# Kernel tuning notes

Hardware: AMD Instinct MI355X
Metric: run time of the kernel (lower is better)

Reference implementation:

```python
import jax, jax.numpy as jnp
import numpy as np

FP8_MAX = 448.0  # e4m3
EPS = 1e-12


def setup_inputs() -> dict:
    key = jax.random.key(0)
    k1, k2, k3 = jax.random.split(key, 3)
    x = jax.random.normal(k1, (4, 4096, 2048), dtype=jnp.float32)
    weight = jax.random.normal(k2, (2048, 2048), dtype=jnp.float32) * 0.02
    bias = jax.random.normal(k3, (2048,), dtype=jnp.float32) * 0.01
    return {"x": x, "weight": weight, "bias": bias}


def reference(x, weight, bias):
    # Per-tensor input quantization (fake FP8 e4m3)
    input_amax = jnp.max(jnp.abs(x))
    input_scale = jnp.maximum(input_amax / FP8_MAX, EPS)
    x_q = jnp.round(jnp.clip(x / input_scale, -FP8_MAX, FP8_MAX))

    # Per-output-channel weight quantization (margin = 0.0 default)
    w_amax = jnp.max(jnp.abs(weight), axis=1)              # [out]
    w_scale = jnp.maximum(w_amax / FP8_MAX, EPS)            # [out]
    w_q = jnp.round(jnp.clip(weight / w_scale[:, None], -FP8_MAX, FP8_MAX))

    # GEMM on quantized values, then dequantize with combined scales
    out_q = jnp.einsum('bsi,oi->bso', x_q, w_q)             # [b, s, out]
    out = out_q * (input_scale * w_scale)                   # broadcast over out
    return out + bias
```

## Files before the change

### kernel.cpp

```cpp
#include <hip/hip_runtime.h>
#include <cstdint>
#include <cstddef>

#define FP8_MAX 448.0f
#define KDIM 2048
#define NDIM 2048

typedef _Float16 half8 __attribute__((ext_vector_type(8)));
typedef float floatx4 __attribute__((ext_vector_type(4)));

__device__ __forceinline__ float fabs4max(float4 v) {
  return fmaxf(fmaxf(fabsf(v.x), fabsf(v.y)), fmaxf(fabsf(v.z), fabsf(v.w)));
}

__device__ __forceinline__ _Float16 quant1(float v, float inv) {
  return (_Float16)rintf(fminf(fmaxf(v * inv, -FP8_MAX), FP8_MAX));
}

__device__ __forceinline__ void gload_lds16(const void* g, void* l) {
  __builtin_amdgcn_global_load_lds(
      (const __attribute__((address_space(1))) unsigned int*)g,
      (__attribute__((address_space(3))) unsigned int*)l,
      16, 0, 0);
}

__global__ __launch_bounds__(256) void k_amax(const float4* __restrict__ x4, int n4,
                                              float* __restrict__ partial) {
  float m = 0.f;
  int stride = gridDim.x * blockDim.x;
  for (int i = blockIdx.x * blockDim.x + threadIdx.x; i < n4; i += stride)
    m = fmaxf(m, fabs4max(x4[i]));
#pragma unroll
  for (int off = 32; off > 0; off >>= 1)
    m = fmaxf(m, __shfl_xor(m, off));
  __shared__ float red[4];
  if ((threadIdx.x & 63) == 0) red[threadIdx.x >> 6] = m;
  __syncthreads();
  if (threadIdx.x == 0)
    partial[blockIdx.x] = fmaxf(fmaxf(red[0], red[1]), fmaxf(red[2], red[3]));
}

__global__ __launch_bounds__(256) void k_amax2(const float* __restrict__ partial, int n,
                                               float* __restrict__ amax) {
  int t = threadIdx.x;
  float m = 0.f;
  for (int i = t; i < n; i += 256) m = fmaxf(m, partial[i]);
#pragma unroll
  for (int off = 32; off > 0; off >>= 1)
    m = fmaxf(m, __shfl_xor(m, off));
  __shared__ float red[4];
  if ((t & 63) == 0) red[t >> 6] = m;
  __syncthreads();
  if (t == 0) amax[0] = fmaxf(fmaxf(red[0], red[1]), fmaxf(red[2], red[3]));
}

__global__ __launch_bounds__(256) void k_xquant(const float4* __restrict__ x4,
                                                const float* __restrict__ amax,
                                                half8* __restrict__ xq, int n8) {
  float scale = fmaxf(amax[0] / FP8_MAX, 1e-12f);
  float inv = 1.f / scale;
  int stride = gridDim.x * blockDim.x;
  for (int i = blockIdx.x * blockDim.x + threadIdx.x; i < n8; i += stride) {
    float4 a = x4[2 * i];
    float4 b = x4[2 * i + 1];
    half8 q;
    q[0] = quant1(a.x, inv); q[1] = quant1(a.y, inv);
    q[2] = quant1(a.z, inv); q[3] = quant1(a.w, inv);
    q[4] = quant1(b.x, inv); q[5] = quant1(b.y, inv);
    q[6] = quant1(b.z, inv); q[7] = quant1(b.w, inv);
    xq[i] = q;
  }
}

__global__ __launch_bounds__(256) void k_wquant(const float* __restrict__ w,
                                                const float* __restrict__ amax,
                                                _Float16* __restrict__ wq,
                                                float* __restrict__ comb) {
  int row = blockIdx.x;
  int t = threadIdx.x;
  const float4* w4 = (const float4*)(w + (size_t)row * KDIM);
  float4 a = w4[2 * t];
  float4 b = w4[2 * t + 1];
  float m = fmaxf(fabs4max(a), fabs4max(b));
#pragma unroll
  for (int off = 32; off > 0; off >>= 1)
    m = fmaxf(m, __shfl_xor(m, off));
  __shared__ float red[4];
  if ((t & 63) == 0) red[t >> 6] = m;
  __syncthreads();
  float rowmax = fmaxf(fmaxf(red[0], red[1]), fmaxf(red[2], red[3]));
  float wscale = fmaxf(rowmax / FP8_MAX, 1e-12f);
  float inv = 1.f / wscale;
  half8 q;
  q[0] = quant1(a.x, inv); q[1] = quant1(a.y, inv);
  q[2] = quant1(a.z, inv); q[3] = quant1(a.w, inv);
  q[4] = quant1(b.x, inv); q[5] = quant1(b.y, inv);
  q[6] = quant1(b.z, inv); q[7] = quant1(b.w, inv);
  *(half8*)(wq + (size_t)row * KDIM + t * 8) = q;
  if (t == 0) {
    float iscale = fmaxf(amax[0] / FP8_MAX, 1e-12f);
    comb[row] = iscale * wscale;
  }
}

__global__ __launch_bounds__(512, 2) void k_gemm256(const _Float16* __restrict__ A,
                                                    const _Float16* __restrict__ B,
                                                    const float* __restrict__ comb,
                                                    const float* __restrict__ bias,
                                                    float* __restrict__ C, int M) {
  __shared__ _Float16 smem[3 * 16384];

  const int NT = KDIM / 32;
  int nwg = gridDim.x;
  int bid = blockIdx.x;
  int swz = bid;
  if ((nwg & 7) == 0) {
    int cpx = nwg >> 3;
    swz = (bid & 7) * cpx + (bid >> 3);
  }
  const int NBN = NDIM / 256;
  int bm = swz / NBN, bn = swz % NBN;

  int tid = threadIdx.x;
  int lane = tid & 63;
  int w = tid >> 6;
  int wr = w >> 2;
  int wc = w & 3;

  int sR = tid >> 2;
  int sc = (tid & 3) ^ ((tid >> 3) & 3);
  const _Float16* gA = A + (size_t)bm * 256 * KDIM;
  const _Float16* gB = B + (size_t)bn * 256 * KDIM;
  size_t off0 = (size_t)sR * KDIM + sc * 8;
  size_t off1 = (size_t)(sR + 128) * KDIM + sc * 8;

  int g = lane >> 4;
  int lr = lane & 15;
  int gx = g ^ ((lr >> 1) & 3);
  int aOff = (wr * 128 + lr) * 64 + gx * 16;
  int bOff = (wc * 64 + lr) * 64 + gx * 16;

  const floatx4 zero4 = {0.f, 0.f, 0.f, 0.f};
  floatx4 acc[8][4];
#pragma unroll
  for (int i = 0; i < 8; ++i)
#pragma unroll
    for (int j = 0; j < 4; ++j) acc[i][j] = zero4;

#define STAGE_A(t, buf)                                                        \
  do {                                                                         \
    const _Float16* src = gA + (size_t)(t)*32;                                 \
    char* dst = (char*)smem + (buf)*32768;                                     \
    gload_lds16(src + off0, dst + tid * 16);                                   \
    gload_lds16(src + off1, dst + 8192 + tid * 16);                            \
  } while (0)
#define STAGE_B(t, buf)                                                        \
  do {                                                                         \
    const _Float16* src = gB + (size_t)(t)*32;                                 \
    char* dst = (char*)smem + (buf)*32768 + 16384;                             \
    gload_lds16(src + off0, dst + tid * 16);                                   \
    gload_lds16(src + off1, dst + 8192 + tid * 16);                            \
  } while (0)

  STAGE_A(0, 0); STAGE_B(0, 0);
  STAGE_A(1, 1); STAGE_B(1, 1);
  asm volatile("s_waitcnt vmcnt(4)" ::: "memory");
  __builtin_amdgcn_s_barrier();

  half8 af[4], bf[4];
  for (int t = 0; t < NT; ++t) {
    int buf = t % 3;
    const char* Abuf = (const char*)smem + buf * 32768;
    const char* Bbuf = Abuf + 16384;
    int nbuf = (t + 2) % 3;
    bool do_stage = (t + 2 < NT);

#pragma unroll
    for (int n = 0; n < 4; ++n) bf[n] = *(const half8*)(Bbuf + bOff + n * 1024);
#pragma unroll
    for (int m = 0; m < 4; ++m) af[m] = *(const half8*)(Abuf + aOff + m * 1024);
    if (do_stage) STAGE_A(t + 2, nbuf);
    __builtin_amdgcn_s_setprio(1);
#pragma unroll
    for (int m = 0; m < 4; ++m)
#pragma unroll
      for (int n = 0; n < 4; ++n)
        acc[m][n] = __builtin_amdgcn_mfma_f32_16x16x32_f16(af[m], bf[n], acc[m][n], 0, 0, 0);
    __builtin_amdgcn_s_setprio(0);
    __builtin_amdgcn_s_barrier();

#pragma unroll
    for (int m = 0; m < 4; ++m) af[m] = *(const half8*)(Abuf + aOff + 4096 + m * 1024);
    if (do_stage) STAGE_B(t + 2, nbuf);
    __builtin_amdgcn_s_setprio(1);
#pragma unroll
    for (int m = 0; m < 4; ++m)
#pragma unroll
      for (int n = 0; n < 4; ++n)
        acc[4 + m][n] = __builtin_amdgcn_mfma_f32_16x16x32_f16(af[m], bf[n], acc[4 + m][n], 0, 0, 0);
    __builtin_amdgcn_s_setprio(0);

    asm volatile("s_waitcnt lgkmcnt(0)" ::: "memory");
    if (t < NT - 2)
      asm volatile("s_waitcnt vmcnt(4)" ::: "memory");
    else
      asm volatile("s_waitcnt vmcnt(0)" ::: "memory");
    __builtin_amdgcn_s_barrier();
  }
#undef STAGE_A
#undef STAGE_B

  int cbase = bn * 256 + wc * 64 + (lane & 15);
  float s[4], bv[4];
#pragma unroll
  for (int n = 0; n < 4; ++n) {
    s[n] = comb[cbase + n * 16];
    bv[n] = bias[cbase + n * 16];
  }
#pragma unroll
  for (int mh = 0; mh < 2; ++mh)
#pragma unroll
    for (int m = 0; m < 4; ++m) {
      size_t row = (size_t)bm * 256 + wr * 128 + mh * 64 + m * 16 + ((lane >> 4) << 2);
      float* cp = C + row * NDIM + cbase;
#pragma unroll
      for (int n = 0; n < 4; ++n)
#pragma unroll
        for (int j = 0; j < 4; ++j)
          cp[n * 16 + (size_t)j * NDIM] = acc[mh * 4 + m][n][j] * s[n] + bv[n];
    }
}

extern "C" void kernel_launch(void* const* d_in, const int* in_sizes, int n_in,
                              void* d_out, int out_size, void* d_ws, size_t ws_size,
                              hipStream_t stream) {
  const float* x = (const float*)d_in[0];
  const float* w = (const float*)d_in[1];
  const float* bias = (const float*)d_in[2];
  float* out = (float*)d_out;
  int M = in_sizes[0] / KDIM;

  char* ws = (char*)d_ws;
  size_t xq_bytes = (size_t)in_sizes[0] * sizeof(_Float16);
  size_t wq_bytes = (size_t)in_sizes[1] * sizeof(_Float16);
  _Float16* xq = (_Float16*)ws;
  _Float16* wq = (_Float16*)(ws + xq_bytes);
  float* comb = (float*)(ws + xq_bytes + wq_bytes);
  float* amax = (float*)(ws + xq_bytes + wq_bytes + 8192);
  float* partial = (float*)(ws + xq_bytes + wq_bytes + 8192 + 256);

  const int AMAX_BLOCKS = 2048;
  int n4 = in_sizes[0] / 4;
  k_amax<<<AMAX_BLOCKS, 256, 0, stream>>>((const float4*)x, n4, partial);
  k_amax2<<<1, 256, 0, stream>>>(partial, AMAX_BLOCKS, amax);

  int n8 = in_sizes[0] / 8;
  k_xquant<<<2048, 256, 0, stream>>>((const float4*)x, amax, (half8*)xq, n8);

  k_wquant<<<NDIM, 256, 0, stream>>>(w, amax, wq, comb);

  int grid = (M / 256) * (NDIM / 256);
  k_gemm256<<<grid, 512, 0, stream>>>(xq, wq, comb, bias, out, M);
}
```

Baseline: 388.8 us.

## Restructure GEMM main loop to K=64 double-buffered half-tile pipeline

```diff
diff --git a/kernel.cpp b/kernel.cpp
--- a/kernel.cpp
+++ b/kernel.cpp
@@ -8,6 +8,8 @@
 
 typedef _Float16 half8 __attribute__((ext_vector_type(8)));
 typedef float floatx4 __attribute__((ext_vector_type(4)));
+
+#define BARRIER() asm volatile("s_barrier" ::: "memory")
 
 __device__ __forceinline__ float fabs4max(float4 v) {
   return fmaxf(fmaxf(fabsf(v.x), fabsf(v.y)), fmaxf(fabsf(v.z), fabsf(v.w)));
@@ -108,9 +110,9 @@
                                                     const float* __restrict__ comb,
                                                     const float* __restrict__ bias,
                                                     float* __restrict__ C, int M) {
-  __shared__ _Float16 smem[3 * 16384];
-
-  const int NT = KDIM / 32;
+  __shared__ _Float16 smem[65536];
+
+  const int NT = KDIM / 64;
   int nwg = gridDim.x;
   int bid = blockIdx.x;
   int swz = bid;
@@ -137,8 +139,8 @@
   int g = lane >> 4;
   int lr = lane & 15;
   int gx = g ^ ((lr >> 1) & 3);
-  int aOff = (wr * 128 + lr) * 64 + gx * 16;
-  int bOff = (wc * 64 + lr) * 64 + gx * 16;
+  int aBase = (wr * 128 + lr) * 64 + gx * 16;
+  int bBase = 32768 + (wc * 64 + lr) * 64 + gx * 16;
 
   const floatx4 zero4 = {0.f, 0.f, 0.f, 0.f};
   floatx4 acc[8][4];
@@ -147,39 +149,44 @@
 #pragma unroll
     for (int j = 0; j < 4; ++j) acc[i][j] = zero4;
 
-#define STAGE_A(t, buf)                                                        \
+#define STAGE_AH(t, kh, bufp)                                                  \
   do {                                                                         \
-    const _Float16* src = gA + (size_t)(t)*32;                                 \
-    char* dst = (char*)smem + (buf)*32768;                                     \
-    gload_lds16(src + off0, dst + tid * 16);                                   \
-    gload_lds16(src + off1, dst + 8192 + tid * 16);                            \
+    const _Float16* s_ = gA + (size_t)(t) * 64 + (kh) * 32;                    \
+    char* d_ = (bufp) + (kh) * 16384;                                          \
+    gload_lds16(s_ + off0, d_ + tid * 16);                                     \
+    gload_lds16(s_ + off1, d_ + 8192 + tid * 16);                              \
   } while (0)
-#define STAGE_B(t, buf)                                                        \
+#define STAGE_BH(t, kh, bufp)                                                  \
   do {                                                                         \
-    const _Float16* src = gB + (size_t)(t)*32;                                 \
-    char* dst = (char*)smem + (buf)*32768 + 16384;                             \
-    gload_lds16(src + off0, dst + tid * 16);                                   \
-    gload_lds16(src + off1, dst + 8192 + tid * 16);                            \
+    const _Float16* s_ = gB + (size_t)(t) * 64 + (kh) * 32;                    \
+    char* d_ = (bufp) + 32768 + (kh) * 16384;                                  \
+    gload_lds16(s_ + off0, d_ + tid * 16);                                     \
+    gload_lds16(s_ + off1, d_ + 8192 + tid * 16);                              \
   } while (0)
 
-  STAGE_A(0, 0); STAGE_B(0, 0);
-  STAGE_A(1, 1); STAGE_B(1, 1);
-  asm volatile("s_waitcnt vmcnt(4)" ::: "memory");
-  __builtin_amdgcn_s_barrier();
+  {
+    char* b0 = (char*)smem;
+    char* b1 = b0 + 65536;
+    STAGE_AH(0, 0, b0); STAGE_BH(0, 0, b0);
+    STAGE_AH(0, 1, b0); STAGE_BH(0, 1, b0);
+    STAGE_AH(1, 0, b1); STAGE_BH(1, 0, b1);
+  }
+  asm volatile("s_waitcnt vmcnt(8)" ::: "memory");
+  BARRIER();
 
   half8 af[4], bf[4];
   for (int t = 0; t < NT; ++t) {
-    int buf = t % 3;
-    const char* Abuf = (const char*)smem + buf * 32768;
-    const char* Bbuf = Abuf + 16384;
-    int nbuf = (t + 2) % 3;
-    bool do_stage = (t + 2 < NT);
-
-#pragma unroll
-    for (int n = 0; n < 4; ++n) bf[n] = *(const half8*)(Bbuf + bOff + n * 1024);
-#pragma unroll
-    for (int m = 0; m < 4; ++m) af[m] = *(const half8*)(Abuf + aOff + m * 1024);
-    if (do_stage) STAGE_A(t + 2, nbuf);
+    char* bufp = (char*)smem + (size_t)(t & 1) * 65536;
+    char* nbufp = (char*)smem + (size_t)((t + 1) & 1) * 65536;
+    bool s01 = (t + 1 < NT);
+    bool s23 = (t + 2 < NT);
+
+#pragma unroll
+    for (int n = 0; n < 4; ++n) bf[n] = *(const half8*)(bufp + bBase + n * 1024);
+#pragma unroll
+    for (int m = 0; m < 4; ++m) af[m] = *(const half8*)(bufp + aBase + m * 1024);
+    if (s01) STAGE_AH(t + 1, 1, nbufp);
+    BARRIER();
     __builtin_amdgcn_s_setprio(1);
 #pragma unroll
     for (int m = 0; m < 4; ++m)
@@ -187,11 +194,12 @@
       for (int n = 0; n < 4; ++n)
         acc[m][n] = __builtin_amdgcn_mfma_f32_16x16x32_f16(af[m], bf[n], acc[m][n], 0, 0, 0);
     __builtin_amdgcn_s_setprio(0);
-    __builtin_amdgcn_s_barrier();
-
-#pragma unroll
-    for (int m = 0; m < 4; ++m) af[m] = *(const half8*)(Abuf + aOff + 4096 + m * 1024);
-    if (do_stage) STAGE_B(t + 2, nbuf);
+    BARRIER();
+
+#pragma unroll
+    for (int m = 0; m < 4; ++m) af[m] = *(const half8*)(bufp + aBase + (4 + m) * 1024);
+    if (s01) STAGE_BH(t + 1, 1, nbufp);
+    BARRIER();
     __builtin_amdgcn_s_setprio(1);
 #pragma unroll
     for (int m = 0; m < 4; ++m)
@@ -199,16 +207,44 @@
       for (int n = 0; n < 4; ++n)
         acc[4 + m][n] = __builtin_amdgcn_mfma_f32_16x16x32_f16(af[m], bf[n], acc[4 + m][n], 0, 0, 0);
     __builtin_amdgcn_s_setprio(0);
-
-    asm volatile("s_waitcnt lgkmcnt(0)" ::: "memory");
-    if (t < NT - 2)
-      asm volatile("s_waitcnt vmcnt(4)" ::: "memory");
+    if (t == NT - 1)
+      asm volatile("s_waitcnt vmcnt(0)" ::: "memory");
     else
-      asm volatile("s_waitcnt vmcnt(0)" ::: "memory");
-    __builtin_amdgcn_s_barrier();
-  }
-#undef STAGE_A
-#undef STAGE_B
+      asm volatile("s_waitcnt vmcnt(8)" ::: "memory");
+    BARRIER();
+
+#pragma unroll
+    for (int n = 0; n < 4; ++n) bf[n] = *(const half8*)(bufp + bBase + 16384 + n * 1024);
+#pragma unroll
+    for (int m = 0; m < 4; ++m) af[m] = *(const half8*)(bufp + aBase + 16384 + m * 1024);
+    if (s23) STAGE_AH(t + 2, 0, bufp);
+    BARRIER();
+    __builtin_amdgcn_s_setprio(1);
+#pragma unroll
+    for (int m = 0; m < 4; ++m)
+#pragma unroll
+      for (int n = 0; n < 4; ++n)
+        acc[m][n] = __builtin_amdgcn_mfma_f32_16x16x32_f16(af[m], bf[n], acc[m][n], 0, 0, 0);
+    __builtin_amdgcn_s_setprio(0);
+    BARRIER();
+
+#pragma unroll
+    for (int m = 0; m < 4; ++m) af[m] = *(const half8*)(bufp + aBase + 16384 + (4 + m) * 1024);
+    if (s23) STAGE_BH(t + 2, 0, bufp);
+    BARRIER();
+    __builtin_amdgcn_s_setprio(1);
+#pragma unroll
+    for (int m = 0; m < 4; ++m)
+#pragma unroll
+      for (int n = 0; n < 4; ++n)
+        acc[4 + m][n] = __builtin_amdgcn_mfma_f32_16x16x32_f16(af[m], bf[n], acc[4 + m][n], 0, 0, 0);
+    __builtin_amdgcn_s_setprio(0);
+    if (t < NT - 1)
+      asm volatile("s_waitcnt vmcnt(8)" ::: "memory");
+    BARRIER();
+  }
+#undef STAGE_AH
+#undef STAGE_BH
 
   int cbase = bn * 256 + wc * 64 + (lane & 15);
   float s[4], bv[4];
```

After: 390.7 us. No clear change (+0.5%).
